# Optimization experiments

Hardware: AMD Instinct MI355X
Metric: run time of the kernel (lower is better)

Reference implementation:

```python
import jax, jax.numpy as jnp
import numpy as np

NUM_NODES = 100000
NUM_RELS = 500
DIM = 64          # input_dim == hidden_dim == output_dim
NUM_EDGES = 1_000_000
LEAKY_SLOPE = 0.01  # torch F.leaky_relu default


def _linear_params(key, fin, fout):
    # torch nn.Linear default init: U(-1/sqrt(fin), 1/sqrt(fin))
    kw, kb = jax.random.split(key)
    s = 1.0 / np.sqrt(fin)
    W = jax.random.uniform(kw, (fout, fin), minval=-s, maxval=s, dtype=jnp.float32)
    b = jax.random.uniform(kb, (fout,), minval=-s, maxval=s, dtype=jnp.float32)
    return W, b


def setup_inputs() -> dict:
    key = jax.random.key(0)
    ks = jax.random.split(key, 12)
    src_idx = jax.random.randint(ks[0], (NUM_EDGES,), 0, NUM_NODES, dtype=jnp.int32)
    dst_idx = jax.random.randint(ks[1], (NUM_EDGES,), 0, NUM_NODES, dtype=jnp.int32)
    rel_idx = jax.random.randint(ks[2], (NUM_EDGES,), 0, NUM_RELS, dtype=jnp.int32)
    ent_embed = jax.random.normal(ks[3], (NUM_NODES, DIM), dtype=jnp.float32)
    rel_embed = jax.random.normal(ks[4], (NUM_RELS, DIM), dtype=jnp.float32)
    W_ent, b_ent = _linear_params(ks[5], DIM, DIM)          # fc_ent
    W_relL, b_relL = _linear_params(ks[6], DIM, DIM)        # fc_rel
    W_rel2, b_rel2 = _linear_params(ks[7], DIM, DIM)        # fc_rel2
    W_rel3, b_rel3 = _linear_params(ks[8], 3 * DIM, DIM)    # fc_rel3
    W_a, b_a = _linear_params(ks[9], DIM, 1)                # a
    W_fc, b_fc = _linear_params(ks[10], 3 * DIM, DIM)       # fc
    return {
        "ent_embed": ent_embed, "rel_embed": rel_embed,
        "W_ent": W_ent, "b_ent": b_ent,
        "W_relL": W_relL, "b_relL": b_relL,
        "W_rel2": W_rel2, "b_rel2": b_rel2,
        "W_rel3": W_rel3, "b_rel3": b_rel3,
        "W_a": W_a, "b_a": b_a,
        "W_fc": W_fc, "b_fc": b_fc,
        "src_idx": src_idx, "dst_idx": dst_idx, "rel_idx": rel_idx,
    }


def reference(ent_embed, rel_embed, W_ent, b_ent, W_relL, b_relL,
              W_rel2, b_rel2, W_rel3, b_rel3, W_a, b_a, W_fc, b_fc,
              src_idx, dst_idx, rel_idx):
    # --- per-edge projections (first=True path: lookup from learned tables) ---
    src = ent_embed[src_idx] @ W_ent.T + b_ent            # [E, D]
    dst = ent_embed[dst_idx] @ W_ent.T + b_ent            # [E, D]
    rel = rel_embed[rel_idx] @ W_relL.T + b_relL          # [E, D]

    # --- edge message c and unnormalized attention b ---
    c = jnp.concatenate([src, dst, rel], axis=1) @ W_fc.T + b_fc   # [E, D]
    logits = jax.nn.leaky_relu((c @ W_a.T + b_a)[:, 0], LEAKY_SLOPE)  # [E]
    b = jnp.exp(logits)                                    # [E] (original uses plain exp)

    # --- scatter-softmax over edges grouped by source node ---
    b_sum = jax.ops.segment_sum(b, src_idx, num_segments=NUM_NODES)  # [N]
    alpha = b / b_sum[src_idx]                             # [E]

    # --- attention-weighted neighbor aggregation ---
    h_ent = jax.ops.segment_sum(alpha[:, None] * c, src_idx,
                                num_segments=NUM_NODES)    # [N, D]

    # --- relation pooling: mean over edges of each relation ---
    rel2 = rel @ W_rel2.T + b_rel2                         # [E, D]
    feats = jnp.concatenate([h_ent[src_idx], h_ent[dst_idx], rel2], axis=1)  # [E, 3D]
    sums = jax.ops.segment_sum(feats, rel_idx, num_segments=NUM_RELS)        # [R, 3D]
    counts = jax.ops.segment_sum(jnp.ones_like(b), rel_idx, num_segments=NUM_RELS)
    mean = sums / jnp.maximum(counts, 1.0)[:, None]        # [R, 3D]

    h_rel = mean @ W_rel3.T + b_rel3                       # [R, D]
    return (h_ent, h_rel)
```

## Files before the change

kernel.cpp:

```cpp
#include <hip/hip_runtime.h>
#include <math.h>

#define N_NODES 100000
#define N_RELS  500
#define DIM     64
#define N_EDGES 1000000
#define SLOPE   0.01f
#define RSUB    16
#define SC_EDGES 2048
#define NB_E    489
#define NBKT    196
#define BSH     9
#define NROWS   (N_RELS + NBKT)
#define BMAX    5632

__global__ void k_fold(const float* __restrict__ W_ent, const float* __restrict__ b_ent,
                       const float* __restrict__ W_relL, const float* __restrict__ b_relL,
                       const float* __restrict__ W_rel2, const float* __restrict__ b_rel2,
                       const float* __restrict__ W_fc, const float* __restrict__ b_fc,
                       float* __restrict__ Wcat, float* __restrict__ dcat,
                       float* __restrict__ MW, float* __restrict__ MQ,
                       float* __restrict__ dW, float* __restrict__ dQ) {
    int idx = blockIdx.x * 256 + threadIdx.x;
    if (idx < 8192) {
        int k = idx >> 7;
        int j2 = idx & 127;
        int jj = j2 & 63;
        int off = (j2 >> 6) * 64;
        float s = 0.f;
        for (int i = 0; i < 64; i++) s += W_fc[jj*192 + off + i] * W_ent[i*64 + k];
        Wcat[k*128 + j2] = s;
    } else if (idx < 12288) {
        int rem = idx - 8192;
        int j = rem >> 6, i = rem & 63;
        float s = 0.f;
        for (int k = 0; k < 64; k++) s += W_fc[j*192 + 128 + k] * W_relL[k*64 + i];
        MW[j*64 + i] = s;
    } else if (idx < 16384) {
        int rem = idx - 12288;
        int j = rem >> 6, i = rem & 63;
        float s = 0.f;
        for (int k = 0; k < 64; k++) s += W_rel2[j*64 + k] * W_relL[k*64 + i];
        MQ[j*64 + i] = s;
    } else if (idx < 16512) {
        int j2 = idx - 16384;
        int jj = j2 & 63;
        int off = (j2 >> 6) * 64;
        float s = 0.f;
        for (int i = 0; i < 64; i++) s += b_ent[i] * W_fc[jj*192 + off + i];
        dcat[j2] = s;
    } else if (idx < 16640) {
        int rem = idx - 16512;
        int vec = rem >> 6, j = rem & 63;
        if (vec == 0) {
            float s = b_fc[j];
            for (int k = 0; k < 64; k++) s += b_relL[k] * W_fc[j*192 + 128 + k];
            dW[j] = s;
        } else {
            float s = b_rel2[j];
            for (int k = 0; k < 64; k++) s += b_relL[k] * W_rel2[j*64 + k];
            dQ[j] = s;
        }
    }
}

__global__ __launch_bounds__(256) void k_node(const float* __restrict__ ent,
        const float* __restrict__ Wcat, const float* __restrict__ dcat,
        const float* __restrict__ W_a,
        float* __restrict__ Uout, float* __restrict__ V,
        float* __restrict__ us, float* __restrict__ vs) {
    __shared__ float sA[64][68];
    __shared__ float sW[64][128];
    int t = threadIdx.x;
    int tile0 = blockIdx.x * 64;
    for (int i = t; i < 2048; i += 256)
        ((float4*)sW)[i] = ((const float4*)Wcat)[i];
    for (int f = t; f < 1024; f += 256) {
        int n = f >> 4, k4 = f & 15;
        float4 v4 = (tile0 + n < N_NODES)
            ? ((const float4*)(ent + (size_t)(tile0 + n) * 64))[k4]
            : make_float4(0.f, 0.f, 0.f, 0.f);
        *(float4*)&sA[n][k4 * 4] = v4;
    }
    __syncthreads();

    int ng = t >> 4;
    int jg = t & 15;
    int n0 = ng * 4;
    int j0 = jg * 8;

    float4 d0 = *(const float4*)(dcat + j0);
    float4 d1 = *(const float4*)(dcat + j0 + 4);
    float acc[4][8];
    #pragma unroll
    for (int a = 0; a < 4; a++) {
        acc[a][0] = d0.x; acc[a][1] = d0.y; acc[a][2] = d0.z; acc[a][3] = d0.w;
        acc[a][4] = d1.x; acc[a][5] = d1.y; acc[a][6] = d1.z; acc[a][7] = d1.w;
    }

    #pragma unroll 4
    for (int k = 0; k < 64; k++) {
        float4 w0 = *(const float4*)&sW[k][j0];
        float4 w1 = *(const float4*)&sW[k][j0 + 4];
        float e0 = sA[n0][k], e1 = sA[n0+1][k], e2 = sA[n0+2][k], e3 = sA[n0+3][k];
        float e[4] = {e0, e1, e2, e3};
        #pragma unroll
        for (int a = 0; a < 4; a++) {
            acc[a][0] += e[a] * w0.x; acc[a][1] += e[a] * w0.y;
            acc[a][2] += e[a] * w0.z; acc[a][3] += e[a] * w0.w;
            acc[a][4] += e[a] * w1.x; acc[a][5] += e[a] * w1.y;
            acc[a][6] += e[a] * w1.z; acc[a][7] += e[a] * w1.w;
        }
    }

    int jw = j0 & 63;
    float4 wa0 = *(const float4*)(W_a + jw);
    float4 wa1 = *(const float4*)(W_a + jw + 4);
    float part[4];
    #pragma unroll
    for (int a = 0; a < 4; a++) {
        part[a] = acc[a][0]*wa0.x + acc[a][1]*wa0.y + acc[a][2]*wa0.z + acc[a][3]*wa0.w
                + acc[a][4]*wa1.x + acc[a][5]*wa1.y + acc[a][6]*wa1.z + acc[a][7]*wa1.w;
    }
    #pragma unroll
    for (int m = 1; m <= 4; m <<= 1) {
        #pragma unroll
        for (int a = 0; a < 4; a++) part[a] += __shfl_xor(part[a], m, 64);
    }
    if ((jg & 7) == 0) {
        float* sv = (jg < 8) ? us : vs;
        #pragma unroll
        for (int a = 0; a < 4; a++)
            if (tile0 + n0 + a < N_NODES) sv[tile0 + n0 + a] = part[a];
    }

    #pragma unroll
    for (int a = 0; a < 4; a++) {
        int n = tile0 + n0 + a;
        if (n >= N_NODES) break;
        float4 o0 = make_float4(acc[a][0], acc[a][1], acc[a][2], acc[a][3]);
        float4 o1 = make_float4(acc[a][4], acc[a][5], acc[a][6], acc[a][7]);
        float* base = (jg < 8) ? (Uout + (size_t)n * 64 + j0) : (V + (size_t)n * 64 + (j0 - 64));
        *(float4*)(base) = o0;
        *(float4*)(base + 4) = o1;
    }
}

__global__ __launch_bounds__(256, 2) void k_relproj(const float* __restrict__ relE,
        const float* __restrict__ MW, const float* __restrict__ MQ,
        const float* __restrict__ dW, const float* __restrict__ dQ,
        const float* __restrict__ W_a,
        float* __restrict__ Wr, float* __restrict__ Qr, float* __restrict__ wsr) {
    int lane = threadIdx.x & 63;
    int wv = threadIdx.x >> 6;
    float mw[64], mq[64];
    #pragma unroll
    for (int i = 0; i < 64; i++) { mw[i] = MW[lane*64 + i]; mq[i] = MQ[lane*64 + i]; }
    float dw = dW[lane], dq = dQ[lane], wa = W_a[lane];
    int r = blockIdx.x * 4 + wv;
    if (r >= N_RELS) return;
    float e = relE[(size_t)r * 64 + lane];
    float w = dw, q = dq;
    #pragma unroll
    for (int i = 0; i < 64; i++) {
        float ei = __shfl(e, i, 64);
        w += ei * mw[i];
        q += ei * mq[i];
    }
    Wr[(size_t)r * 64 + lane] = w;
    Qr[(size_t)r * 64 + lane] = q;
    float tw = w * wa;
    #pragma unroll
    for (int o = 32; o; o >>= 1) tw += __shfl_xor(tw, o, 64);
    if (lane == 0) wsr[r] = tw;
}

__global__ void k_zero(int* __restrict__ a, int n) {
    int g = blockIdx.x * 256 + threadIdx.x;
    if (g < n) a[g] = 0;
}

__global__ __launch_bounds__(256) void k_hist(const int* __restrict__ src, const int* __restrict__ rel,
        int* __restrict__ cnt_rel, int* __restrict__ bucket_cnt, int* __restrict__ blkhist) {
    __shared__ int lcntR[N_RELS];
    __shared__ int lcntS[NBKT];
    int t = threadIdx.x;
    for (int r = t; r < N_RELS; r += 256) lcntR[r] = 0;
    for (int b = t; b < NBKT; b += 256) lcntS[b] = 0;
    __syncthreads();
    int base = blockIdx.x * SC_EDGES;
    if (base + SC_EDGES <= N_EDGES) {
        int e0 = base + t * 8;
        int4 sa = *(const int4*)(src + e0);
        int4 sb = *(const int4*)(src + e0 + 4);
        int4 ra = *(const int4*)(rel + e0);
        int4 rb = *(const int4*)(rel + e0 + 4);
        atomicAdd(&lcntS[sa.x >> BSH], 1); atomicAdd(&lcntS[sa.y >> BSH], 1);
        atomicAdd(&lcntS[sa.z >> BSH], 1); atomicAdd(&lcntS[sa.w >> BSH], 1);
        atomicAdd(&lcntS[sb.x >> BSH], 1); atomicAdd(&lcntS[sb.y >> BSH], 1);
        atomicAdd(&lcntS[sb.z >> BSH], 1); atomicAdd(&lcntS[sb.w >> BSH], 1);
        atomicAdd(&lcntR[ra.x], 1); atomicAdd(&lcntR[ra.y], 1);
        atomicAdd(&lcntR[ra.z], 1); atomicAdd(&lcntR[ra.w], 1);
        atomicAdd(&lcntR[rb.x], 1); atomicAdd(&lcntR[rb.y], 1);
        atomicAdd(&lcntR[rb.z], 1); atomicAdd(&lcntR[rb.w], 1);
    } else {
        for (int g = base + t; g < N_EDGES; g += 256) {
            atomicAdd(&lcntS[src[g] >> BSH], 1);
            atomicAdd(&lcntR[rel[g]], 1);
        }
    }
    __syncthreads();
    for (int r = t; r < N_RELS; r += 256) {
        int c = lcntR[r];
        blkhist[(size_t)r * NB_E + blockIdx.x] = c;
        if (c) atomicAdd(&cnt_rel[r], c);
    }
    for (int b = t; b < NBKT; b += 256) {
        int c = lcntS[b];
        blkhist[(size_t)(N_RELS + b) * NB_E + blockIdx.x] = c;
        if (c) atomicAdd(&bucket_cnt[b], c);
    }
}

__global__ void k_scan_two(const int* __restrict__ cnt_rel, const int* __restrict__ bucket_cnt,
                           int* __restrict__ starts) {
    __shared__ int tot[256];
    int t = threadIdx.x;
    const int* cnt = blockIdx.x ? bucket_cnt : cnt_rel;
    int n = blockIdx.x ? NBKT : N_RELS;
    int* out = starts + (blockIdx.x ? N_RELS : 0);
    int myv[4];
    int mySum = 0;
    for (int q = 0; q < 4; q++) {
        int g = t * 4 + q;
        int v = (g < n) ? cnt[g] : 0;
        myv[q] = v; mySum += v;
    }
    tot[t] = mySum;
    __syncthreads();
    for (int o = 1; o < 256; o <<= 1) {
        int u = (t >= o) ? tot[t - o] : 0;
        __syncthreads();
        tot[t] += u;
        __syncthreads();
    }
    int run = tot[t] - mySum;
    for (int q = 0; q < 4; q++) {
        int g = t * 4 + q;
        if (g < n) out[g] = run;
        run += myv[q];
    }
}

__global__ __launch_bounds__(256) void k_scan_relblk(const int* __restrict__ starts,
        const int* __restrict__ blkhist, int* __restrict__ blkbase) {
    int lane = threadIdx.x & 63;
    int row = (blockIdx.x * 256 + threadIdx.x) >> 6;
    if (row >= NROWS) return;
    int run = starts[row];
    for (int base = 0; base < NB_E; base += 64) {
        int b = base + lane;
        int v = (b < NB_E) ? blkhist[(size_t)row * NB_E + b] : 0;
        int x = v;
        #pragma unroll
        for (int o = 1; o < 64; o <<= 1) {
            int y = __shfl_up(x, o, 64);
            if (lane >= o) x += y;
        }
        if (b < NB_E) blkbase[(size_t)row * NB_E + b] = run + (x - v);
        run += __shfl(x, 63, 64);
    }
}

__global__ __launch_bounds__(256) void k_scatter(const int* __restrict__ src, const int* __restrict__ dst,
        const int* __restrict__ rel, const int* __restrict__ blkbase,
        int2* __restrict__ pay_rel, int* __restrict__ stg_a, int* __restrict__ stg_b) {
    __shared__ int lbaseR[N_RELS];
    __shared__ int loffR[N_RELS];
    __shared__ int lbaseS[NBKT];
    __shared__ int loffS[NBKT];
    int t = threadIdx.x;
    for (int r = t; r < N_RELS; r += 256) {
        lbaseR[r] = blkbase[(size_t)r * NB_E + blockIdx.x];
        loffR[r] = 0;
    }
    for (int b = t; b < NBKT; b += 256) {
        lbaseS[b] = blkbase[(size_t)(N_RELS + b) * NB_E + blockIdx.x];
        loffS[b] = 0;
    }
    __syncthreads();
    int base = blockIdx.x * SC_EDGES;
    if (base + SC_EDGES <= N_EDGES) {
        int e0 = base + t * 8;
        int4 sa = *(const int4*)(src + e0);
        int4 sb = *(const int4*)(src + e0 + 4);
        int4 da = *(const int4*)(dst + e0);
        int4 db = *(const int4*)(dst + e0 + 4);
        int4 ra = *(const int4*)(rel + e0);
        int4 rb = *(const int4*)(rel + e0 + 4);
        int s[8] = {sa.x, sa.y, sa.z, sa.w, sb.x, sb.y, sb.z, sb.w};
        int d[8] = {da.x, da.y, da.z, da.w, db.x, db.y, db.z, db.w};
        int r8[8] = {ra.x, ra.y, ra.z, ra.w, rb.x, rb.y, rb.z, rb.w};
        int p[8], q[8];
        #pragma unroll
        for (int j = 0; j < 8; j++) q[j] = lbaseR[r8[j]] + atomicAdd(&loffR[r8[j]], 1);
        #pragma unroll
        for (int j = 0; j < 8; j++) p[j] = lbaseS[s[j] >> BSH] + atomicAdd(&loffS[s[j] >> BSH], 1);
        #pragma unroll
        for (int j = 0; j < 8; j++) pay_rel[q[j]] = make_int2(s[j], d[j]);
        #pragma unroll
        for (int j = 0; j < 8; j++) stg_a[p[j]] = d[j];
        #pragma unroll
        for (int j = 0; j < 8; j++) stg_b[p[j]] = ((s[j] & 511) << 9) | r8[j];
    } else {
        for (int g = base + t; g < N_EDGES; g += 256) {
            int s = src[g], d = dst[g], r = rel[g];
            int q = lbaseR[r] + atomicAdd(&loffR[r], 1);
            pay_rel[q] = make_int2(s, d);
            int sb2 = s >> BSH;
            int p = lbaseS[sb2] + atomicAdd(&loffS[sb2], 1);
            stg_a[p] = d;
            stg_b[p] = ((s & 511) << 9) | r;
        }
    }
}

__global__ __launch_bounds__(256) void k_sortb(const int* __restrict__ stg_a,
        const int* __restrict__ stg_b, const int* __restrict__ starts,
        const int* __restrict__ bucket_cnt, int2* __restrict__ pay_src,
        int* __restrict__ start_src, int* __restrict__ cnt_src) {
    __shared__ int hist[512];
    __shared__ int lstart[512];
    __shared__ int loff[512];
    __shared__ int tot[256];
    __shared__ int2 lpay[BMAX];
    int bkt = blockIdx.x;
    int base = starts[N_RELS + bkt];
    int n = bucket_cnt[bkt];
    int t = threadIdx.x;
    hist[t] = 0; hist[t + 256] = 0;
    __syncthreads();
    for (int i = t; i < n; i += 256)
        atomicAdd(&hist[stg_b[base + i] >> 9], 1);
    __syncthreads();
    int v0 = hist[t * 2], v1 = hist[t * 2 + 1];
    int mySum = v0 + v1;
    tot[t] = mySum;
    __syncthreads();
    for (int o = 1; o < 256; o <<= 1) {
        int u = (t >= o) ? tot[t - o] : 0;
        __syncthreads();
        tot[t] += u;
        __syncthreads();
    }
    int run = tot[t] - mySum;
    lstart[t * 2] = run;
    lstart[t * 2 + 1] = run + v0;
    loff[t * 2] = 0;
    loff[t * 2 + 1] = 0;
    int node0 = bkt * 512 + t * 2;
    if (node0 < N_NODES) { start_src[node0] = base + run; cnt_src[node0] = v0; }
    if (node0 + 1 < N_NODES) { start_src[node0 + 1] = base + run + v0; cnt_src[node0 + 1] = v1; }
    __syncthreads();
    bool fits = (n <= BMAX);
    for (int i = t; i < n; i += 256) {
        int bb = stg_b[base + i];
        int d = stg_a[base + i];
        int lo = bb >> 9;
        int2 pr = make_int2(d, bb & 511);
        int pos = lstart[lo] + atomicAdd(&loff[lo], 1);
        if (fits) lpay[pos] = pr;
        else pay_src[base + pos] = pr;
    }
    __syncthreads();
    if (fits)
        for (int i = t; i < n; i += 256)
            pay_src[base + i] = lpay[i];
}

__global__ __launch_bounds__(256) void k_attn(const int2* __restrict__ pay,
        const int* __restrict__ start_src, const int* __restrict__ cnt_src,
        const float* __restrict__ us, const float* __restrict__ vs,
        const float* __restrict__ wsr, const float* __restrict__ V,
        const float* __restrict__ Wr, const float* __restrict__ b_a_p,
        float* __restrict__ h) {
    int lane = threadIdx.x & 63;
    int wv = threadIdx.x >> 6;
    int n = blockIdx.x * 4 + wv;
    if (n >= N_NODES) return;
    int st = start_src[n];
    int cnt = cnt_src[n];
    if (cnt == 0) { h[(size_t)n * 64 + lane] = 0.f; return; }
    float ba = b_a_p[0];
    float usn = us[n];

    if (cnt <= 64) {
        int2 pe = (lane < cnt) ? pay[st + lane] : make_int2(0, 0);
        float bexp = 0.f;
        if (lane < cnt) {
            float s = usn + vs[pe.x] + wsr[pe.y] + ba;
            s = s > 0.f ? s : SLOPE * s;
            bexp = expf(s);
        }
        float bp = bexp;
        #pragma unroll
        for (int o = 32; o; o >>= 1) bp += __shfl_xor(bp, o, 64);
        float inv = 1.f / bp;
        int sub = lane >> 3;
        int li = lane & 7;
        float4 a0 = make_float4(0.f, 0.f, 0.f, 0.f);
        float4 a1 = make_float4(0.f, 0.f, 0.f, 0.f);
        int groups = (cnt + 7) >> 3;
        for (int g = 0; g < groups; g++) {
            int esel = 8 * g + sub;
            float be = __shfl(bexp, esel, 64);
            int de = __shfl(pe.x, esel, 64);
            int re = __shfl(pe.y, esel, 64);
            const float* vb = V + (size_t)de * 64 + li * 8;
            const float* wb = Wr + (size_t)re * 64 + li * 8;
            float4 v0 = *(const float4*)vb;
            float4 v1 = *(const float4*)(vb + 4);
            float4 w0 = *(const float4*)wb;
            float4 w1 = *(const float4*)(wb + 4);
            a0.x += be * (v0.x + w0.x); a0.y += be * (v0.y + w0.y);
            a0.z += be * (v0.z + w0.z); a0.w += be * (v0.w + w0.w);
            a1.x += be * (v1.x + w1.x); a1.y += be * (v1.y + w1.y);
            a1.z += be * (v1.z + w1.z); a1.w += be * (v1.w + w1.w);
        }
        #pragma unroll
        for (int m = 8; m <= 32; m <<= 1) {
            a0.x += __shfl_xor(a0.x, m, 64); a0.y += __shfl_xor(a0.y, m, 64);
            a0.z += __shfl_xor(a0.z, m, 64); a0.w += __shfl_xor(a0.w, m, 64);
            a1.x += __shfl_xor(a1.x, m, 64); a1.y += __shfl_xor(a1.y, m, 64);
            a1.z += __shfl_xor(a1.z, m, 64); a1.w += __shfl_xor(a1.w, m, 64);
        }
        if (lane < 8) {
            float* hp = h + (size_t)n * 64 + lane * 8;
            float4 u0 = *(const float4*)hp;
            float4 u1 = *(const float4*)(hp + 4);
            float4 o0 = make_float4(u0.x + a0.x * inv, u0.y + a0.y * inv,
                                    u0.z + a0.z * inv, u0.w + a0.w * inv);
            float4 o1 = make_float4(u1.x + a1.x * inv, u1.y + a1.y * inv,
                                    u1.z + a1.z * inv, u1.w + a1.w * inv);
            *(float4*)hp = o0;
            *(float4*)(hp + 4) = o1;
        }
        return;
    }

    float bp = 0.f;
    for (int k = lane; k < cnt; k += 64) {
        int2 p = pay[st + k];
        float s = usn + vs[p.x] + wsr[p.y] + ba;
        s = s > 0.f ? s : SLOPE * s;
        bp += expf(s);
    }
    #pragma unroll
    for (int o = 32; o; o >>= 1) bp += __shfl_xor(bp, o, 64);
    float inv = 1.f / bp;
    float acc = 0.f;
    for (int k = 0; k < cnt; k++) {
        int2 p = pay[st + k];
        float s = usn + vs[p.x] + wsr[p.y] + ba;
        s = s > 0.f ? s : SLOPE * s;
        float b = expf(s);
        acc += b * (V[(size_t)p.x * 64 + lane] + Wr[(size_t)p.y * 64 + lane]);
    }
    float u = h[(size_t)n * 64 + lane];
    h[(size_t)n * 64 + lane] = u + acc * inv;
}

__global__ __launch_bounds__(256) void k_relpool(const int2* __restrict__ pay,
        const int* __restrict__ start_rel, const int* __restrict__ cnt_rel,
        const float* __restrict__ h, float* __restrict__ acc_rel) {
    int r = blockIdx.x / RSUB;
    int sub = blockIdx.x % RSUB;
    int st = start_rel[r];
    int cnt = cnt_rel[r];
    int t = threadIdx.x;
    int j = t >> 5;
    int side = (t >> 4) & 1;
    int li = t & 15;

    int chunk = (cnt + RSUB - 1) / RSUB;
    int k0 = sub * chunk;
    int k1 = min(k0 + chunk, cnt);
    int len = k1 - k0;

    float4 acc = make_float4(0.f, 0.f, 0.f, 0.f);
    if (len > 0) {
        int steps = (len + 15) >> 4;
        int mA = j, mB = j + 8;
        bool vA = mA < len, vB = mB < len;
        int2 pA = vA ? pay[st + k0 + mA] : make_int2(0, 0);
        int2 pB = vB ? pay[st + k0 + mB] : make_int2(0, 0);
        for (int it = 0; it < steps; it++) {
            int nA = mA + 16, nB = mB + 16;
            bool wA = (it + 1 < steps) && (nA < len);
            bool wB = (it + 1 < steps) && (nB < len);
            int2 qA = wA ? pay[st + k0 + nA] : make_int2(0, 0);
            int2 qB = wB ? pay[st + k0 + nB] : make_int2(0, 0);
            int idxA = side ? pA.y : pA.x;
            int idxB = side ? pB.y : pB.x;
            float4 hA = *(const float4*)(h + (size_t)idxA * 64 + li * 4);
            float4 hB = *(const float4*)(h + (size_t)idxB * 64 + li * 4);
            if (vA) { acc.x += hA.x; acc.y += hA.y; acc.z += hA.z; acc.w += hA.w; }
            if (vB) { acc.x += hB.x; acc.y += hB.y; acc.z += hB.z; acc.w += hB.w; }
            pA = qA; pB = qB; mA = nA; mB = nB; vA = wA; vB = wB;
        }
    }
    __shared__ float4 red[256];
    red[t] = acc;
    __syncthreads();
    if (t < 128) {
        float4 a = red[t], b = red[t + 128];
        a.x += b.x; a.y += b.y; a.z += b.z; a.w += b.w;
        red[t] = a;
    }
    __syncthreads();
    if (t < 64) {
        float4 a = red[t], b = red[t + 64];
        a.x += b.x; a.y += b.y; a.z += b.z; a.w += b.w;
        red[t] = a;
    }
    __syncthreads();
    if (t < 32) {
        float4 a = red[t], b = red[t + 32];
        a.x += b.x; a.y += b.y; a.z += b.z; a.w += b.w;
        float* dstp = &acc_rel[r * 128 + side * 64 + li * 4];
        atomicAdd(dstp + 0, a.x);
        atomicAdd(dstp + 1, a.y);
        atomicAdd(dstp + 2, a.z);
        atomicAdd(dstp + 3, a.w);
    }
}

__global__ void k_relfin(const float* __restrict__ acc_rel, const int* __restrict__ cnt_rel,
                         const float* __restrict__ Qr, const float* __restrict__ W_rel3,
                         const float* __restrict__ b_rel3, float* __restrict__ out) {
    int g = blockIdx.x * 256 + threadIdx.x;
    if (g >= N_RELS * 64) return;
    int r = g >> 6;
    int j = g & 63;
    int cnt = cnt_rel[r];
    float invc = 1.f / (float)(cnt > 0 ? cnt : 1);
    float s = b_rel3[j];
    for (int k = 0; k < 128; k++) s += acc_rel[r * 128 + k] * invc * W_rel3[j * 192 + k];
    if (cnt > 0)
        for (int k = 0; k < 64; k++) s += Qr[r * 64 + k] * W_rel3[j * 192 + 128 + k];
    out[g] = s;
}

extern "C" void kernel_launch(void* const* d_in, const int* in_sizes, int n_in,
                              void* d_out, int out_size, void* d_ws, size_t ws_size,
                              hipStream_t stream) {
    const float* ent    = (const float*)d_in[0];
    const float* relE   = (const float*)d_in[1];
    const float* W_ent  = (const float*)d_in[2];
    const float* b_ent  = (const float*)d_in[3];
    const float* W_relL = (const float*)d_in[4];
    const float* b_relL = (const float*)d_in[5];
    const float* W_rel2 = (const float*)d_in[6];
    const float* b_rel2 = (const float*)d_in[7];
    const float* W_rel3 = (const float*)d_in[8];
    const float* b_rel3 = (const float*)d_in[9];
    const float* W_a    = (const float*)d_in[10];
    const float* b_a    = (const float*)d_in[11];
    const float* W_fc   = (const float*)d_in[12];
    const float* b_fc   = (const float*)d_in[13];
    const int* src = (const int*)d_in[14];
    const int* dst = (const int*)d_in[15];
    const int* rel = (const int*)d_in[16];
    float* out = (float*)d_out;

    char* ws = (char*)d_ws;
    size_t off = 0;
    auto alloc = [&](size_t bytes) -> void* {
        void* p = ws + off;
        off += (bytes + 255) & ~(size_t)255;
        return p;
    };
    float* Wcat = (float*)alloc(8192 * 4);
    float* dcat = (float*)alloc(128 * 4);
    float* MW  = (float*)alloc(4096 * 4);
    float* MQ  = (float*)alloc(4096 * 4);
    float* dW  = (float*)alloc(64 * 4);
    float* dQ  = (float*)alloc(64 * 4);
    float* V   = (float*)alloc((size_t)N_NODES * 64 * 4);
    float* us  = (float*)alloc((size_t)N_NODES * 4);
    float* vs  = (float*)alloc((size_t)N_NODES * 4);
    float* Wr  = (float*)alloc((size_t)N_RELS * 64 * 4);
    float* Qr  = (float*)alloc((size_t)N_RELS * 64 * 4);
    float* wsr = (float*)alloc((size_t)N_RELS * 4);
    int* cnt_src   = (int*)alloc((size_t)N_NODES * 4);
    int* start_src = (int*)alloc((size_t)N_NODES * 4);
    int* cnts      = (int*)alloc((size_t)NROWS * 4);
    int* starts    = (int*)alloc((size_t)NROWS * 4);
    int* blkhist   = (int*)alloc((size_t)NROWS * NB_E * 4);
    int* blkbase   = (int*)alloc((size_t)NROWS * NB_E * 4);
    int* stg_a     = (int*)alloc((size_t)N_EDGES * 4);
    int* stg_b     = (int*)alloc((size_t)N_EDGES * 4);
    int2* pay_src  = (int2*)alloc((size_t)N_EDGES * 8);
    int2* pay_rel  = (int2*)alloc((size_t)N_EDGES * 8);
    float* acc_rel = (float*)alloc((size_t)N_RELS * 128 * 4);

    int* cnt_rel    = cnts;
    int* bucket_cnt = cnts + N_RELS;

    k_zero<<<(NROWS + 255) / 256, 256, 0, stream>>>(cnts, NROWS);
    k_zero<<<(N_RELS * 128 + 255) / 256, 256, 0, stream>>>((int*)acc_rel, N_RELS * 128);

    k_fold<<<65, 256, 0, stream>>>(W_ent, b_ent, W_relL, b_relL, W_rel2, b_rel2,
                                   W_fc, b_fc, Wcat, dcat, MW, MQ, dW, dQ);
    k_node<<<(N_NODES + 63) / 64, 256, 0, stream>>>(ent, Wcat, dcat, W_a, out, V, us, vs);
    k_relproj<<<125, 256, 0, stream>>>(relE, MW, MQ, dW, dQ, W_a, Wr, Qr, wsr);
    k_hist<<<NB_E, 256, 0, stream>>>(src, rel, cnt_rel, bucket_cnt, blkhist);
    k_scan_two<<<2, 256, 0, stream>>>(cnt_rel, bucket_cnt, starts);
    k_scan_relblk<<<(NROWS * 64) / 256, 256, 0, stream>>>(starts, blkhist, blkbase);
    k_scatter<<<NB_E, 256, 0, stream>>>(src, dst, rel, blkbase, pay_rel, stg_a, stg_b);
    k_sortb<<<NBKT, 256, 0, stream>>>(stg_a, stg_b, starts, bucket_cnt,
                                      pay_src, start_src, cnt_src);
    k_attn<<<N_NODES / 4, 256, 0, stream>>>(pay_src, start_src, cnt_src,
                                            us, vs, wsr, V, Wr, b_a, out);
    k_relpool<<<N_RELS * RSUB, 256, 0, stream>>>(pay_rel, starts, cnt_rel, out, acc_rel);
    k_relfin<<<(N_RELS * 64 + 255) / 256, 256, 0, stream>>>(acc_rel, cnt_rel, Qr, W_rel3,
                                                            b_rel3, out + (size_t)N_NODES * 64);
}
```

Before: 338.0 us.

## Store gathered node/relation features in bf16 to halve gather traffic

The per-node V projection and the per-relation Wr table are now written as bf16, and k_attn reads them as packed uint4 loads. k_attn also writes a bf16 copy of h_ent, which k_relpool gathers instead of the fp32 output, with its thread mapping widened to 8 elements per lane. This halves the bytes moved by the random gathers in the attention and relation-pooling stages. In exchange it loses precision in the aggregated values and adds an extra bf16 store of h.

```diff
diff --git a/kernel.cpp b/kernel.cpp
--- a/kernel.cpp
+++ b/kernel.cpp
@@ -13,6 +13,14 @@
 #define BSH     9
 #define NROWS   (N_RELS + NBKT)
 #define BMAX    5632
+
+__device__ __forceinline__ unsigned short f2bf(float f) {
+    unsigned int u = __float_as_uint(f);
+    u += 0x7FFFu + ((u >> 16) & 1u);
+    return (unsigned short)(u >> 16);
+}
+__device__ __forceinline__ float bfl(unsigned int u) { return __uint_as_float(u << 16); }
+__device__ __forceinline__ float bfh(unsigned int u) { return __uint_as_float(u & 0xFFFF0000u); }
 
 __global__ void k_fold(const float* __restrict__ W_ent, const float* __restrict__ b_ent,
                        const float* __restrict__ W_relL, const float* __restrict__ b_relL,
@@ -67,7 +75,7 @@
 __global__ __launch_bounds__(256) void k_node(const float* __restrict__ ent,
         const float* __restrict__ Wcat, const float* __restrict__ dcat,
         const float* __restrict__ W_a,
-        float* __restrict__ Uout, float* __restrict__ V,
+        float* __restrict__ Uout, unsigned short* __restrict__ V16,
         float* __restrict__ us, float* __restrict__ vs) {
     __shared__ float sA[64][68];
     __shared__ float sW[64][128];
@@ -138,11 +146,20 @@
     for (int a = 0; a < 4; a++) {
         int n = tile0 + n0 + a;
         if (n >= N_NODES) break;
-        float4 o0 = make_float4(acc[a][0], acc[a][1], acc[a][2], acc[a][3]);
-        float4 o1 = make_float4(acc[a][4], acc[a][5], acc[a][6], acc[a][7]);
-        float* base = (jg < 8) ? (Uout + (size_t)n * 64 + j0) : (V + (size_t)n * 64 + (j0 - 64));
-        *(float4*)(base) = o0;
-        *(float4*)(base + 4) = o1;
+        if (jg < 8) {
+            float4 o0 = make_float4(acc[a][0], acc[a][1], acc[a][2], acc[a][3]);
+            float4 o1 = make_float4(acc[a][4], acc[a][5], acc[a][6], acc[a][7]);
+            float* base = Uout + (size_t)n * 64 + j0;
+            *(float4*)(base) = o0;
+            *(float4*)(base + 4) = o1;
+        } else {
+            uint4 pv;
+            pv.x = (unsigned int)f2bf(acc[a][0]) | ((unsigned int)f2bf(acc[a][1]) << 16);
+            pv.y = (unsigned int)f2bf(acc[a][2]) | ((unsigned int)f2bf(acc[a][3]) << 16);
+            pv.z = (unsigned int)f2bf(acc[a][4]) | ((unsigned int)f2bf(acc[a][5]) << 16);
+            pv.w = (unsigned int)f2bf(acc[a][6]) | ((unsigned int)f2bf(acc[a][7]) << 16);
+            *(uint4*)(V16 + (size_t)n * 64 + (j0 - 64)) = pv;
+        }
     }
 }
 
@@ -150,7 +167,7 @@
         const float* __restrict__ MW, const float* __restrict__ MQ,
         const float* __restrict__ dW, const float* __restrict__ dQ,
         const float* __restrict__ W_a,
-        float* __restrict__ Wr, float* __restrict__ Qr, float* __restrict__ wsr) {
+        unsigned short* __restrict__ Wr16, float* __restrict__ Qr, float* __restrict__ wsr) {
     int lane = threadIdx.x & 63;
     int wv = threadIdx.x >> 6;
     float mw[64], mq[64];
@@ -167,7 +184,7 @@
         w += ei * mw[i];
         q += ei * mq[i];
     }
-    Wr[(size_t)r * 64 + lane] = w;
+    Wr16[(size_t)r * 64 + lane] = f2bf(w);
     Qr[(size_t)r * 64 + lane] = q;
     float tw = w * wa;
     #pragma unroll
@@ -381,16 +398,20 @@
 __global__ __launch_bounds__(256) void k_attn(const int2* __restrict__ pay,
         const int* __restrict__ start_src, const int* __restrict__ cnt_src,
         const float* __restrict__ us, const float* __restrict__ vs,
-        const float* __restrict__ wsr, const float* __restrict__ V,
-        const float* __restrict__ Wr, const float* __restrict__ b_a_p,
-        float* __restrict__ h) {
+        const float* __restrict__ wsr, const unsigned short* __restrict__ V16,
+        const unsigned short* __restrict__ Wr16, const float* __restrict__ b_a_p,
+        float* __restrict__ h, unsigned short* __restrict__ h16) {
     int lane = threadIdx.x & 63;
     int wv = threadIdx.x >> 6;
     int n = blockIdx.x * 4 + wv;
     if (n >= N_NODES) return;
     int st = start_src[n];
     int cnt = cnt_src[n];
-    if (cnt == 0) { h[(size_t)n * 64 + lane] = 0.f; return; }
+    if (cnt == 0) {
+        h[(size_t)n * 64 + lane] = 0.f;
+        if (lane < 8) *(uint4*)(h16 + (size_t)n * 64 + lane * 8) = make_uint4(0,0,0,0);
+        return;
+    }
     float ba = b_a_p[0];
     float usn = us[n];
 
@@ -408,42 +429,40 @@
         float inv = 1.f / bp;
         int sub = lane >> 3;
         int li = lane & 7;
-        float4 a0 = make_float4(0.f, 0.f, 0.f, 0.f);
-        float4 a1 = make_float4(0.f, 0.f, 0.f, 0.f);
+        float a[8] = {0.f,0.f,0.f,0.f,0.f,0.f,0.f,0.f};
         int groups = (cnt + 7) >> 3;
         for (int g = 0; g < groups; g++) {
             int esel = 8 * g + sub;
             float be = __shfl(bexp, esel, 64);
             int de = __shfl(pe.x, esel, 64);
             int re = __shfl(pe.y, esel, 64);
-            const float* vb = V + (size_t)de * 64 + li * 8;
-            const float* wb = Wr + (size_t)re * 64 + li * 8;
-            float4 v0 = *(const float4*)vb;
-            float4 v1 = *(const float4*)(vb + 4);
-            float4 w0 = *(const float4*)wb;
-            float4 w1 = *(const float4*)(wb + 4);
-            a0.x += be * (v0.x + w0.x); a0.y += be * (v0.y + w0.y);
-            a0.z += be * (v0.z + w0.z); a0.w += be * (v0.w + w0.w);
-            a1.x += be * (v1.x + w1.x); a1.y += be * (v1.y + w1.y);
-            a1.z += be * (v1.z + w1.z); a1.w += be * (v1.w + w1.w);
+            uint4 vv = *(const uint4*)(V16 + (size_t)de * 64 + li * 8);
+            uint4 ww = *(const uint4*)(Wr16 + (size_t)re * 64 + li * 8);
+            a[0] += be * (bfl(vv.x) + bfl(ww.x)); a[1] += be * (bfh(vv.x) + bfh(ww.x));
+            a[2] += be * (bfl(vv.y) + bfl(ww.y)); a[3] += be * (bfh(vv.y) + bfh(ww.y));
+            a[4] += be * (bfl(vv.z) + bfl(ww.z)); a[5] += be * (bfh(vv.z) + bfh(ww.z));
+            a[6] += be * (bfl(vv.w) + bfl(ww.w)); a[7] += be * (bfh(vv.w) + bfh(ww.w));
         }
         #pragma unroll
         for (int m = 8; m <= 32; m <<= 1) {
-            a0.x += __shfl_xor(a0.x, m, 64); a0.y += __shfl_xor(a0.y, m, 64);
-            a0.z += __shfl_xor(a0.z, m, 64); a0.w += __shfl_xor(a0.w, m, 64);
-            a1.x += __shfl_xor(a1.x, m, 64); a1.y += __shfl_xor(a1.y, m, 64);
-            a1.z += __shfl_xor(a1.z, m, 64); a1.w += __shfl_xor(a1.w, m, 64);
+            #pragma unroll
+            for (int d = 0; d < 8; d++) a[d] += __shfl_xor(a[d], m, 64);
         }
         if (lane < 8) {
             float* hp = h + (size_t)n * 64 + lane * 8;
-            float4 u0 = *(const float4*)hp;
-            float4 u1 = *(const float4*)(hp + 4);
-            float4 o0 = make_float4(u0.x + a0.x * inv, u0.y + a0.y * inv,
-                                    u0.z + a0.z * inv, u0.w + a0.w * inv);
-            float4 o1 = make_float4(u1.x + a1.x * inv, u1.y + a1.y * inv,
-                                    u1.z + a1.z * inv, u1.w + a1.w * inv);
+            float o[8];
+            #pragma unroll
+            for (int d = 0; d < 8; d++) o[d] = hp[d] + a[d] * inv;
+            float4 o0 = make_float4(o[0], o[1], o[2], o[3]);
+            float4 o1 = make_float4(o[4], o[5], o[6], o[7]);
             *(float4*)hp = o0;
             *(float4*)(hp + 4) = o1;
+            uint4 pv;
+            pv.x = (unsigned int)f2bf(o[0]) | ((unsigned int)f2bf(o[1]) << 16);
+            pv.y = (unsigned int)f2bf(o[2]) | ((unsigned int)f2bf(o[3]) << 16);
+            pv.z = (unsigned int)f2bf(o[4]) | ((unsigned int)f2bf(o[5]) << 16);
+            pv.w = (unsigned int)f2bf(o[6]) | ((unsigned int)f2bf(o[7]) << 16);
+            *(uint4*)(h16 + (size_t)n * 64 + lane * 8) = pv;
         }
         return;
     }
@@ -464,74 +483,80 @@
         float s = usn + vs[p.x] + wsr[p.y] + ba;
         s = s > 0.f ? s : SLOPE * s;
         float b = expf(s);
-        acc += b * (V[(size_t)p.x * 64 + lane] + Wr[(size_t)p.y * 64 + lane]);
+        float vv = bfl((unsigned int)V16[(size_t)p.x * 64 + lane] << 16 >> 16 << 16);
+        vv = __uint_as_float((unsigned int)V16[(size_t)p.x * 64 + lane] << 16);
+        float wv2 = __uint_as_float((unsigned int)Wr16[(size_t)p.y * 64 + lane] << 16);
+        acc += b * (vv + wv2);
     }
     float u = h[(size_t)n * 64 + lane];
-    h[(size_t)n * 64 + lane] = u + acc * inv;
+    float o = u + acc * inv;
+    h[(size_t)n * 64 + lane] = o;
+    h16[(size_t)n * 64 + lane] = f2bf(o);
 }
 
 __global__ __launch_bounds__(256) void k_relpool(const int2* __restrict__ pay,
         const int* __restrict__ start_rel, const int* __restrict__ cnt_rel,
-        const float* __restrict__ h, float* __restrict__ acc_rel) {
+        const unsigned short* __restrict__ h16, float* __restrict__ acc_rel) {
     int r = blockIdx.x / RSUB;
     int sub = blockIdx.x % RSUB;
     int st = start_rel[r];
     int cnt = cnt_rel[r];
     int t = threadIdx.x;
-    int j = t >> 5;
-    int side = (t >> 4) & 1;
-    int li = t & 15;
+    int j = t >> 4;
+    int side = (t >> 3) & 1;
+    int li = t & 7;
 
     int chunk = (cnt + RSUB - 1) / RSUB;
     int k0 = sub * chunk;
     int k1 = min(k0 + chunk, cnt);
     int len = k1 - k0;
 
-    float4 acc = make_float4(0.f, 0.f, 0.f, 0.f);
+    float a[8] = {0.f,0.f,0.f,0.f,0.f,0.f,0.f,0.f};
     if (len > 0) {
-        int steps = (len + 15) >> 4;
-        int mA = j, mB = j + 8;
+        int steps = (len + 31) >> 5;
+        int mA = j, mB = j + 16;
         bool vA = mA < len, vB = mB < len;
         int2 pA = vA ? pay[st + k0 + mA] : make_int2(0, 0);
         int2 pB = vB ? pay[st + k0 + mB] : make_int2(0, 0);
         for (int it = 0; it < steps; it++) {
-            int nA = mA + 16, nB = mB + 16;
+            int nA = mA + 32, nB = mB + 32;
             bool wA = (it + 1 < steps) && (nA < len);
             bool wB = (it + 1 < steps) && (nB < len);
             int2 qA = wA ? pay[st + k0 + nA] : make_int2(0, 0);
             int2 qB = wB ? pay[st + k0 + nB] : make_int2(0, 0);
             int idxA = side ? pA.y : pA.x;
             int idxB = side ? pB.y : pB.x;
-            float4 hA = *(const float4*)(h + (size_t)idxA * 64 + li * 4);
-            float4 hB = *(const float4*)(h + (size_t)idxB * 64 + li * 4);
-            if (vA) { acc.x += hA.x; acc.y += hA.y; acc.z += hA.z; acc.w += hA.w; }
-            if (vB) { acc.x += hB.x; acc.y += hB.y; acc.z += hB.z; acc.w += hB.w; }
+            uint4 hA = *(const uint4*)(h16 + (size_t)idxA * 64 + li * 8);
+            uint4 hB = *(const uint4*)(h16 + (size_t)idxB * 64 + li * 8);
+            if (vA) {
+                a[0] += bfl(hA.x); a[1] += bfh(hA.x); a[2] += bfl(hA.y); a[3] += bfh(hA.y);
+                a[4] += bfl(hA.z); a[5] += bfh(hA.z); a[6] += bfl(hA.w); a[7] += bfh(hA.w);
+            }
+            if (vB) {
+                a[0] += bfl(hB.x); a[1] += bfh(hB.x); a[2] += bfl(hB.y); a[3] += bfh(hB.y);
+                a[4] += bfl(hB.z); a[5] += bfh(hB.z); a[6] += bfl(hB.w); a[7] += bfh(hB.w);
+            }
             pA = qA; pB = qB; mA = nA; mB = nB; vA = wA; vB = wB;
         }
     }
-    __shared__ float4 red[256];
-    red[t] = acc;
-    __syncthreads();
-    if (t < 128) {
-        float4 a = red[t], b = red[t + 128];
-        a.x += b.x; a.y += b.y; a.z += b.z; a.w += b.w;
-        red[t] = a;
-    }
-    __syncthreads();
-    if (t < 64) {
-        float4 a = red[t], b = red[t + 64];
-        a.x += b.x; a.y += b.y; a.z += b.z; a.w += b.w;
-        red[t] = a;
-    }
-    __syncthreads();
-    if (t < 32) {
-        float4 a = red[t], b = red[t + 32];
-        a.x += b.x; a.y += b.y; a.z += b.z; a.w += b.w;
-        float* dstp = &acc_rel[r * 128 + side * 64 + li * 4];
-        atomicAdd(dstp + 0, a.x);
-        atomicAdd(dstp + 1, a.y);
-        atomicAdd(dstp + 2, a.z);
-        atomicAdd(dstp + 3, a.w);
+    __shared__ float red[256][8];
+    #pragma unroll
+    for (int d = 0; d < 8; d++) red[t][d] = a[d];
+    __syncthreads();
+    #pragma unroll
+    for (int off = 128; off >= 16; off >>= 1) {
+        if (t < off) {
+            #pragma unroll
+            for (int d = 0; d < 8; d++) red[t][d] += red[t + off][d];
+        }
+        __syncthreads();
+    }
+    if (t < 16) {
+        int sd = (t >> 3) & 1;
+        int ll = t & 7;
+        float* dstp = &acc_rel[r * 128 + sd * 64 + ll * 8];
+        #pragma unroll
+        for (int d = 0; d < 8; d++) atomicAdd(dstp + d, red[t][d]);
     }
 }
 
@@ -586,10 +611,11 @@
     float* MQ  = (float*)alloc(4096 * 4);
     float* dW  = (float*)alloc(64 * 4);
     float* dQ  = (float*)alloc(64 * 4);
-    float* V   = (float*)alloc((size_t)N_NODES * 64 * 4);
+    unsigned short* V16 = (unsigned short*)alloc((size_t)N_NODES * 64 * 2);
+    unsigned short* h16 = (unsigned short*)alloc((size_t)N_NODES * 64 * 2);
     float* us  = (float*)alloc((size_t)N_NODES * 4);
     float* vs  = (float*)alloc((size_t)N_NODES * 4);
-    float* Wr  = (float*)alloc((size_t)N_RELS * 64 * 4);
+    unsigned short* Wr16 = (unsigned short*)alloc((size_t)N_RELS * 64 * 2);
     float* Qr  = (float*)alloc((size_t)N_RELS * 64 * 4);
     float* wsr = (float*)alloc((size_t)N_RELS * 4);
     int* cnt_src   = (int*)alloc((size_t)N_NODES * 4);
@@ -612,17 +638,17 @@
 
     k_fold<<<65, 256, 0, stream>>>(W_ent, b_ent, W_relL, b_relL, W_rel2, b_rel2,
                                    W_fc, b_fc, Wcat, dcat, MW, MQ, dW, dQ);
-    k_node<<<(N_NODES + 63) / 64, 256, 0, stream>>>(ent, Wcat, dcat, W_a, out, V, us, vs);
-    k_relproj<<<125, 256, 0, stream>>>(relE, MW, MQ, dW, dQ, W_a, Wr, Qr, wsr);
+    k_node<<<(N_NODES + 63) / 64, 256, 0, stream>>>(ent, Wcat, dcat, W_a, out, V16, us, vs);
+    k_relproj<<<125, 256, 0, stream>>>(relE, MW, MQ, dW, dQ, W_a, Wr16, Qr, wsr);
     k_hist<<<NB_E, 256, 0, stream>>>(src, rel, cnt_rel, bucket_cnt, blkhist);
     k_scan_two<<<2, 256, 0, stream>>>(cnt_rel, bucket_cnt, starts);
-    k_scan_relblk<<<(NROWS * 64) / 256, 256, 0, stream>>>(starts, blkhist, blkbase);
+    k_scan_relblk<<<(NROWS * 64 + 255) / 256, 256, 0, stream>>>(starts, blkhist, blkbase);
     k_scatter<<<NB_E, 256, 0, stream>>>(src, dst, rel, blkbase, pay_rel, stg_a, stg_b);
     k_sortb<<<NBKT, 256, 0, stream>>>(stg_a, stg_b, starts, bucket_cnt,
                                       pay_src, start_src, cnt_src);
     k_attn<<<N_NODES / 4, 256, 0, stream>>>(pay_src, start_src, cnt_src,
-                                            us, vs, wsr, V, Wr, b_a, out);
-    k_relpool<<<N_RELS * RSUB, 256, 0, stream>>>(pay_rel, starts, cnt_rel, out, acc_rel);
+                                            us, vs, wsr, V16, Wr16, b_a, out, h16);
+    k_relpool<<<N_RELS * RSUB, 256, 0, stream>>>(pay_rel, starts, cnt_rel, h16, acc_rel);
     k_relfin<<<(N_RELS * 64 + 255) / 256, 256, 0, stream>>>(acc_rel, cnt_rel, Qr, W_rel3,
                                                             b_rel3, out + (size_t)N_NODES * 64);
 }
```

Result: faster. 319.4 us (-5.5%).
